# Optimization experiments

Measured on AMD Instinct MI355X. Metric: run time of the kernel, lower is better.

Reference implementation:

```python
import jax, jax.numpy as jnp
import numpy as np

D_MODEL = 1024
SCALE = 1.0 / np.sqrt(D_MODEL)


def setup_inputs() -> dict:
    key = jax.random.key(0)
    ks = jax.random.split(key, 9)
    B, S, D = 4, 2048, D_MODEL
    std = 1.0 / np.sqrt(D)
    x = jax.random.normal(ks[0], (B, S, D), dtype=jnp.float32)
    # nn.Linear weights: [out, in]; we store transposed [in, out] for x @ W
    Wq = jax.random.uniform(ks[1], (D, D), jnp.float32, -std, std)
    bq = jax.random.uniform(ks[2], (D,), jnp.float32, -std, std)
    Wk = jax.random.uniform(ks[3], (D, D), jnp.float32, -std, std)
    bk = jax.random.uniform(ks[4], (D,), jnp.float32, -std, std)
    Wv = jax.random.uniform(ks[5], (D, D), jnp.float32, -std, std)
    bv = jax.random.uniform(ks[6], (D,), jnp.float32, -std, std)
    Wo = jax.random.uniform(ks[7], (D, D), jnp.float32, -std, std)
    bo = jax.random.uniform(ks[8], (D,), jnp.float32, -std, std)
    return {"x": x, "Wq": Wq, "bq": bq, "Wk": Wk, "bk": bk,
            "Wv": Wv, "bv": bv, "Wo": Wo, "bo": bo}


def reference(x, Wq, bq, Wk, bk, Wv, bv, Wo, bo):
    q = x @ Wq + bq                      # [B,S,D]
    k = x @ Wk + bk
    v = x @ Wv + bv
    scores = jnp.einsum('bsd,btd->bst', q, k) * SCALE  # [B,S,S]
    weights = jax.nn.softmax(scores, axis=-1)
    out = jnp.einsum('bst,btd->bsd', weights, v)       # [B,S,D]
    return out @ Wo + bo
```

## Files before the change

### kernel.cpp

```cpp
#include <hip/hip_runtime.h>
#include <hip/hip_bf16.h>
#include <cstdint>

typedef __bf16 bf16x8 __attribute__((ext_vector_type(8)));
typedef float f32x4 __attribute__((ext_vector_type(4)));

__device__ __forceinline__ float bf2f(unsigned short u) {
  union { unsigned int i; float f; } x; x.i = ((unsigned int)u) << 16; return x.f;
}
__device__ __forceinline__ unsigned short f2bf(float f) {
  __hip_bfloat16 h = __float2bfloat16(f);
  return __builtin_bit_cast(unsigned short, h);
}

__device__ __forceinline__ void gload_lds16(const void* g, void* l) {
  auto gp = reinterpret_cast<__attribute__((address_space(1))) char*>(
      reinterpret_cast<uintptr_t>(g));
  auto lp = reinterpret_cast<__attribute__((address_space(3))) char*>(
      reinterpret_cast<uintptr_t>(l));
  __builtin_amdgcn_global_load_lds(gp, lp, 16, 0, 0);
}

#define SB() __builtin_amdgcn_sched_barrier(0)
#define BAR()                         \
  do {                                \
    SB();                             \
    __builtin_amdgcn_s_barrier();     \
    SB();                             \
  } while (0)
#define LGKM0()                                          \
  do {                                                   \
    asm volatile("s_waitcnt lgkmcnt(0)" ::: "memory");   \
    SB();                                                \
  } while (0)

__device__ __forceinline__ void xcd_swz(int& bx, int& by, int& bz) {
  const int gx = gridDim.x, gy = gridDim.y;
  const int n = gx * gy * (int)gridDim.z;
  int lin = blockIdx.x + gx * (blockIdx.y + gy * blockIdx.z);
  lin = (lin & 7) * (n >> 3) + (lin >> 3);
  bx = lin % gx; lin /= gx;
  by = lin % gy; bz = lin / gy;
}

__global__ __launch_bounds__(256) void cvt_f32_to_bf16(
    const float* __restrict__ in, unsigned short* __restrict__ out, long n4) {
  long i = (long)blockIdx.x * 256 + threadIdx.x;
  if (i >= n4) return;
  const float4 v = reinterpret_cast<const float4*>(in)[i];
  ushort4 o;
  o.x = f2bf(v.x); o.y = f2bf(v.y); o.z = f2bf(v.z); o.w = f2bf(v.w);
  reinterpret_cast<ushort4*>(out)[i] = o;
}

__global__ void transpose_w4(const float* __restrict__ w0,
                             const float* __restrict__ w1,
                             const float* __restrict__ w2,
                             const float* __restrict__ w3,
                             unsigned short* __restrict__ out) {
  const int z = blockIdx.z;
  const float* in = (z == 0) ? w0 : (z == 1) ? w1 : (z == 2) ? w2 : w3;
  out += (size_t)z * 1024 * 1024;
  __shared__ float tile[32][33];
  const int c0 = blockIdx.x * 32, r0 = blockIdx.y * 32;
  tile[threadIdx.y][threadIdx.x] =
      in[(size_t)(r0 + threadIdx.y) * 1024 + c0 + threadIdx.x];
  __syncthreads();
  out[(size_t)(c0 + threadIdx.y) * 1024 + r0 + threadIdx.x] =
      f2bf(tile[threadIdx.x][threadIdx.y]);
}

__global__ void concat_bias3(const float* a, const float* b, const float* c,
                             float* o) {
  int i = blockIdx.x * 256 + threadIdx.x;
  if (i >= 3072) return;
  o[i] = (i < 1024) ? a[i] : (i < 2048 ? b[i - 1024] : c[i - 2048]);
}

#define STAGE128(gbase, ld, ldsbase, rowbase)                                 \
  {                                                                           \
    _Pragma("unroll") for (int l_ = 0; l_ < 2; ++l_) {                        \
      const int seg_ = (w << 1) + l_;                                         \
      const int r0_ = (rowbase) + (seg_ << 3);                                \
      const int gr_ = r0_ + (lane >> 3);                                      \
      const int sc_ = ((lane & 7) ^ (lane >> 3)) << 3;                        \
      gload_lds16((gbase) + (size_t)gr_ * (ld) + sc_, (ldsbase) + r0_ * 64);  \
    }                                                                         \
  }

#define LDA_FRAG(dst, tile, rbase)                                            \
  _Pragma("unroll") for (int m_ = 0; m_ < 4; ++m_)                            \
  _Pragma("unroll") for (int kk_ = 0; kk_ < 2; ++kk_) {                       \
    const int row_ = (rbase) + (m_ << 4) + (lane & 15);                       \
    const int ch_ = ((kk_ << 2) + (lane >> 4)) ^ (lane & 7);                  \
    dst[m_][kk_] =                                                            \
        *reinterpret_cast<const bf16x8*>((tile) + row_ * 64 + (ch_ << 3));    \
  }
#define LDB_FRAG(dst, tile, rbase)                                            \
  _Pragma("unroll") for (int n_ = 0; n_ < 2; ++n_)                            \
  _Pragma("unroll") for (int kk_ = 0; kk_ < 2; ++kk_) {                       \
    const int row_ = (rbase) + (n_ << 4) + (lane & 15);                       \
    const int ch_ = ((kk_ << 2) + (lane >> 4)) ^ (lane & 7);                  \
    dst[n_][kk_] =                                                            \
        *reinterpret_cast<const bf16x8*>((tile) + row_ * 64 + (ch_ << 3));    \
  }

#define STAGE_A(gbase, ld, ldsbase, h)                                        \
  {                                                                           \
    _Pragma("unroll") for (int l_ = 0; l_ < 2; ++l_) {                        \
      const int seg_ = (w << 1) + l_;                                         \
      const int r0_ = ((seg_ >> 3) << 7) + ((h) << 6) + ((seg_ & 7) << 3);    \
      const int gr_ = r0_ + (lane >> 3);                                      \
      const int sc_ = ((lane & 7) ^ (lane >> 3)) << 3;                        \
      gload_lds16((gbase) + (size_t)gr_ * (ld) + sc_, (ldsbase) + r0_ * 64);  \
    }                                                                         \
  }
#define STAGE_B(gbase, ld, ldsbase, h)                                        \
  {                                                                           \
    _Pragma("unroll") for (int l_ = 0; l_ < 2; ++l_) {                        \
      const int seg_ = (w << 1) + l_;                                         \
      const int r0_ = ((seg_ >> 2) << 6) + ((h) << 5) + ((seg_ & 3) << 3);    \
      const int gr_ = r0_ + (lane >> 3);                                      \
      const int sc_ = ((lane & 7) ^ (lane >> 3)) << 3;                        \
      gload_lds16((gbase) + (size_t)gr_ * (ld) + sc_, (ldsbase) + r0_ * 64);  \
    }                                                                         \
  }

#define MFMA_QUAD(a_, b_, af_, bf_)                                           \
  __builtin_amdgcn_s_setprio(1);                                              \
  _Pragma("unroll") for (int m_ = 0; m_ < 4; ++m_)                            \
  _Pragma("unroll") for (int n_ = 0; n_ < 2; ++n_)                            \
  _Pragma("unroll") for (int kk_ = 0; kk_ < 2; ++kk_)                         \
      acc[(a_) * 4 + m_][(b_) * 2 + n_] =                                     \
          __builtin_amdgcn_mfma_f32_16x16x32_bf16(                            \
              af_[m_][kk_], bf_[n_][kk_], acc[(a_) * 4 + m_][(b_) * 2 + n_],  \
              0, 0, 0);                                                       \
  __builtin_amdgcn_s_setprio(0);

template <typename OutT, bool HAS_BIAS>
__global__ __launch_bounds__(512, 2) void gemm256(
    const unsigned short* __restrict__ A,
    const unsigned short* __restrict__ Bt,
    OutT* __restrict__ C,
    const float* __restrict__ bias,
    int K, int lda, int ldb, int ldc, float scale,
    long sA, long sB, long sC) {
  int bx, by, bz;
  xcd_swz(bx, by, bz);
  A  += (long)bz * sA;
  Bt += (long)bz * sB;
  C  += (long)bz * sC;
  const int n0 = bx << 8;
  const int m0 = by << 8;
  __shared__ __attribute__((aligned(16))) unsigned short lds[2 * 32768];
  const int t = threadIdx.x;
  const int lane = t & 63;
  const int w = t >> 6;
  const int wm = w >> 2, wn = w & 3;
  const unsigned short* gA = A + (size_t)m0 * lda;
  const unsigned short* gB = Bt + (size_t)n0 * ldb;
  const int NT = K >> 6;

  f32x4 acc[8][4];
  const f32x4 vz = {0.f, 0.f, 0.f, 0.f};
#pragma unroll
  for (int i = 0; i < 8; ++i)
#pragma unroll
    for (int j = 0; j < 4; ++j) acc[i][j] = vz;

  {
    unsigned short* a0 = lds;
    unsigned short* b0t = lds + 16384;
    STAGE_A(gA, lda, a0, 0);
    STAGE_B(gB, ldb, b0t, 0);
    STAGE_B(gB, ldb, b0t, 1);
    STAGE_A(gA, lda, a0, 1);
    if (NT > 1) {
      unsigned short* a1 = lds + 32768;
      unsigned short* b1t = lds + 32768 + 16384;
      STAGE_A(gA + 64, lda, a1, 0);
      STAGE_B(gB + 64, ldb, b1t, 0);
      STAGE_B(gB + 64, ldb, b1t, 1);
      asm volatile("s_waitcnt vmcnt(6)" ::: "memory");
    } else {
      asm volatile("s_waitcnt vmcnt(0)" ::: "memory");
    }
  }
  BAR();

  for (int kt = 0; kt < NT; ++kt) {
    unsigned short* at = lds + ((kt & 1) << 15);
    unsigned short* bt = at + 16384;
    unsigned short* atN = lds + (((kt + 1) & 1) << 15);
    const unsigned short* gA1 = gA + (size_t)(kt + 1) * 64;
    const unsigned short* gA2 = gA + (size_t)(kt + 2) * 64;
    const unsigned short* gB2 = gB + (size_t)(kt + 2) * 64;
    const bool st1 = kt + 1 < NT, st2 = kt + 2 < NT;

    bf16x8 af[4][2], b0[2][2], b1[2][2];

    LDA_FRAG(af, at, (wm << 7));
    LDB_FRAG(b0, bt, (wn << 6));
    if (st1) STAGE_A(gA1, lda, atN, 1);
    BAR();
    LGKM0();
    MFMA_QUAD(0, 0, af, b0);
    BAR();

    LDB_FRAG(b1, bt, (wn << 6) + 32);
    if (st2) STAGE_A(gA2, lda, at, 0);
    BAR();
    LGKM0();
    MFMA_QUAD(0, 1, af, b1);
    BAR();

    LDA_FRAG(af, at, (wm << 7) + 64);
    if (st2) STAGE_B(gB2, ldb, bt, 0);
    BAR();
    LGKM0();
    MFMA_QUAD(1, 0, af, b0);
    BAR();

    if (st2) STAGE_B(gB2, ldb, bt, 1);
    if (kt < NT - 3) {
      asm volatile("s_waitcnt vmcnt(6)" ::: "memory");
    } else {
      asm volatile("s_waitcnt vmcnt(0)" ::: "memory");
    }
    BAR();
    MFMA_QUAD(1, 1, af, b1);
    BAR();
  }

  const int crow0 = m0 + (wm << 7) + ((lane >> 4) << 2);
  const int ccol0 = n0 + (wn << 6) + (lane & 15);
#pragma unroll
  for (int mf = 0; mf < 8; ++mf) {
#pragma unroll
    for (int nf = 0; nf < 4; ++nf) {
      const int col = ccol0 + (nf << 4);
      const float bb = HAS_BIAS ? bias[col] : 0.f;
#pragma unroll
      for (int i = 0; i < 4; ++i) {
        const int row = crow0 + (mf << 4) + i;
        const float v = acc[mf][nf][i] * scale + bb;
        if constexpr (sizeof(OutT) == 2) {
          C[(size_t)row * ldc + col] = (OutT)f2bf(v);
        } else {
          C[(size_t)row * ldc + col] = (OutT)v;
        }
      }
    }
  }
}

#define MFMA_QUAD128(b_, af_, bf_)                                            \
  __builtin_amdgcn_s_setprio(1);                                              \
  _Pragma("unroll") for (int m_ = 0; m_ < 4; ++m_)                            \
  _Pragma("unroll") for (int n_ = 0; n_ < 2; ++n_)                            \
  _Pragma("unroll") for (int kk_ = 0; kk_ < 2; ++kk_)                         \
      acc[m_][(b_) * 2 + n_] = __builtin_amdgcn_mfma_f32_16x16x32_bf16(       \
          af_[m_][kk_], bf_[n_][kk_], acc[m_][(b_) * 2 + n_], 0, 0, 0);       \
  __builtin_amdgcn_s_setprio(0);

template <typename OutT, bool HAS_BIAS, bool VSPLIT>
__global__ __launch_bounds__(512, 2) void gemm128t(
    const unsigned short* __restrict__ A,
    const unsigned short* __restrict__ Bt,
    OutT* __restrict__ C,
    const float* __restrict__ bias,
    unsigned short* __restrict__ vt,
    int K, int lda, int ldb, int ldc, float scale,
    long sA, long sB, long sC) {
  int bx, by, bz;
  xcd_swz(bx, by, bz);
  A  += (long)bz * sA;
  Bt += (long)bz * sB;
  C  += (long)bz * sC;
  const int n0 = bx << 7;
  const int m0 = by << 8;
  __shared__ __attribute__((aligned(16))) unsigned short lds[3 * 24576];
  const int t = threadIdx.x;
  const int lane = t & 63;
  const int w = t >> 6;
  const int wm = w >> 1, wn = w & 1;
  const unsigned short* gA = A + (size_t)m0 * lda;
  const unsigned short* gB = Bt + (size_t)n0 * ldb;
  const int NT = K >> 6;

  f32x4 acc[4][4];
  const f32x4 vz = {0.f, 0.f, 0.f, 0.f};
#pragma unroll
  for (int i = 0; i < 4; ++i)
#pragma unroll
    for (int j = 0; j < 4; ++j) acc[i][j] = vz;

  {
    STAGE128(gA, lda, lds, 0);
    STAGE128(gA, lda, lds, 128);
    STAGE128(gB, ldb, lds + 16384, 0);
    STAGE128(gA + 64, lda, lds + 24576, 0);
    STAGE128(gA + 64, lda, lds + 24576, 128);
    STAGE128(gB + 64, ldb, lds + 24576 + 16384, 0);
    asm volatile("s_waitcnt vmcnt(6)" ::: "memory");
  }
  BAR();

  int idx = 0;
  for (int kt = 0; kt < NT; ++kt) {
    unsigned short* at = lds + idx * 24576;
    unsigned short* btile = at + 16384;
    int idx2 = idx + 2; if (idx2 >= 3) idx2 -= 3;
    unsigned short* st = lds + idx2 * 24576;
    const unsigned short* gA2 = gA + (size_t)(kt + 2) * 64;
    const unsigned short* gB2 = gB + (size_t)(kt + 2) * 64;
    const bool st2 = kt + 2 < NT;

    bf16x8 af[4][2], b0[2][2], b1[2][2];

    LDA_FRAG(af, at, (wm << 6));
    LDB_FRAG(b0, btile, (wn << 6));
    if (st2) {
      STAGE128(gA2, lda, st, 0);
      STAGE128(gA2, lda, st, 128);
    }
    BAR();
    LGKM0();
    MFMA_QUAD128(0, af, b0);
    BAR();

    LDB_FRAG(b1, btile, (wn << 6) + 32);
    if (st2) STAGE128(gB2, ldb, st + 16384, 0);
    if (kt < NT - 2) {
      asm volatile("s_waitcnt vmcnt(6)" ::: "memory");
    } else {
      asm volatile("s_waitcnt vmcnt(0)" ::: "memory");
    }
    BAR();
    LGKM0();
    MFMA_QUAD128(1, af, b1);
    BAR();

    idx = (idx + 1 == 3) ? 0 : idx + 1;
  }

  const int crow0 = m0 + (wm << 6) + ((lane >> 4) << 2);
  const int ccol0 = n0 + (wn << 6) + (lane & 15);

  if (VSPLIT && n0 >= 2048) {
    const int b = m0 >> 11;
#pragma unroll
    for (int mf = 0; mf < 4; ++mf) {
#pragma unroll
      for (int nf = 0; nf < 4; ++nf) {
        const int col = ccol0 + (nf << 4);
        const float bb = HAS_BIAS ? bias[col] : 0.f;
        const int d = col - 2048;
        const int s = (crow0 & 2047) + (mf << 4);
        ushort4 o;
        o.x = f2bf(acc[mf][nf][0] * scale + bb);
        o.y = f2bf(acc[mf][nf][1] * scale + bb);
        o.z = f2bf(acc[mf][nf][2] * scale + bb);
        o.w = f2bf(acc[mf][nf][3] * scale + bb);
        *reinterpret_cast<ushort4*>(vt + (((size_t)b << 10) + d) * 2048 + s) = o;
      }
    }
    return;
  }

#pragma unroll
  for (int mf = 0; mf < 4; ++mf) {
#pragma unroll
    for (int nf = 0; nf < 4; ++nf) {
      const int col = ccol0 + (nf << 4);
      const float bb = HAS_BIAS ? bias[col] : 0.f;
#pragma unroll
      for (int i = 0; i < 4; ++i) {
        const int row = crow0 + (mf << 4) + i;
        const float v = acc[mf][nf][i] * scale + bb;
        if constexpr (sizeof(OutT) == 2) {
          C[(size_t)row * ldc + col] = (OutT)f2bf(v);
        } else {
          C[(size_t)row * ldc + col] = (OutT)v;
        }
      }
    }
  }
}

__global__ __launch_bounds__(256) void softmax_inplace(
    unsigned short* __restrict__ P, int S) {
  const size_t row = blockIdx.x;
  unsigned short* p = P + row * (size_t)S;
  const int t = threadIdx.x;
  const int lane = t & 63, w = t >> 6;
  const uint4 raw = reinterpret_cast<const uint4*>(p)[t];
  unsigned int u[4] = {raw.x, raw.y, raw.z, raw.w};
  float v[8];
#pragma unroll
  for (int j = 0; j < 4; ++j) {
    v[2 * j]     = bf2f((unsigned short)(u[j] & 0xffffu));
    v[2 * j + 1] = bf2f((unsigned short)(u[j] >> 16));
  }
  float mx = v[0];
#pragma unroll
  for (int j = 1; j < 8; ++j) mx = fmaxf(mx, v[j]);
#pragma unroll
  for (int off = 32; off >= 1; off >>= 1) mx = fmaxf(mx, __shfl_xor(mx, off, 64));
  __shared__ float red[4];
  if (lane == 0) red[w] = mx;
  __syncthreads();
  mx = fmaxf(fmaxf(red[0], red[1]), fmaxf(red[2], red[3]));
  float e[8];
  float s = 0.f;
#pragma unroll
  for (int j = 0; j < 8; ++j) { e[j] = __expf(v[j] - mx); s += e[j]; }
#pragma unroll
  for (int off = 32; off >= 1; off >>= 1) s += __shfl_xor(s, off, 64);
  __syncthreads();
  if (lane == 0) red[w] = s;
  __syncthreads();
  s = red[0] + red[1] + red[2] + red[3];
  const float inv = 1.f / s;
  unsigned int o[4];
#pragma unroll
  for (int j = 0; j < 4; ++j)
    o[j] = (unsigned int)f2bf(e[2 * j] * inv) |
           ((unsigned int)f2bf(e[2 * j + 1] * inv) << 16);
  uint4 ov; ov.x = o[0]; ov.y = o[1]; ov.z = o[2]; ov.w = o[3];
  reinterpret_cast<uint4*>(p)[t] = ov;
}

extern "C" void kernel_launch(void* const* d_in, const int* in_sizes, int n_in,
                              void* d_out, int out_size, void* d_ws, size_t ws_size,
                              hipStream_t stream) {
  (void)in_sizes; (void)n_in; (void)out_size; (void)ws_size;
  const float* x  = (const float*)d_in[0];
  const float* Wq = (const float*)d_in[1];
  const float* bq = (const float*)d_in[2];
  const float* Wk = (const float*)d_in[3];
  const float* bk = (const float*)d_in[4];
  const float* Wv = (const float*)d_in[5];
  const float* bv = (const float*)d_in[6];
  const float* Wo = (const float*)d_in[7];
  const float* bo = (const float*)d_in[8];
  float* out = (float*)d_out;

  constexpr int B = 4, S = 2048, D = 1024;
  constexpr long BS = (long)B * S;
  constexpr size_t MB = 1ull << 20;
  char* ws = (char*)d_ws;
  unsigned short* xb   = (unsigned short*)(ws + 0);
  unsigned short* Wall = (unsigned short*)(ws + 16 * MB);
  float*          bqkv = (float*)(ws + 24 * MB);
  unsigned short* QKVc = (unsigned short*)(ws + 25 * MB);
  unsigned short* Vt   = (unsigned short*)(ws + 57 * MB);
  unsigned short* Sc   = (unsigned short*)(ws + 73 * MB);
  unsigned short* AO   = (unsigned short*)(ws + 0);

  const float scale = 0.03125f;

  cvt_f32_to_bf16<<<(BS * D / 4 + 255) / 256, 256, 0, stream>>>(x, xb, BS * D / 4);
  transpose_w4<<<dim3(32, 32, 4), dim3(32, 32), 0, stream>>>(Wq, Wk, Wv, Wo, Wall);
  concat_bias3<<<12, 256, 0, stream>>>(bq, bk, bv, bqkv);

  gemm128t<unsigned short, true, true><<<dim3(24, 32, 1), 512, 0, stream>>>(
      xb, Wall, QKVc, bqkv, Vt, D, D, D, 2048, 1.f, 0, 0, 0);

  gemm256<unsigned short, false><<<dim3(S / 256, S / 256, B), 512, 0, stream>>>(
      QKVc + 0, QKVc + 1024, Sc, nullptr, D, 2048, 2048, S, scale,
      (long)S * 2048, (long)S * 2048, (long)S * S);

  softmax_inplace<<<B * S, 256, 0, stream>>>(Sc, S);

  gemm128t<unsigned short, false, false><<<dim3(8, 8, 4), 512, 0, stream>>>(
      Sc, Vt, AO, nullptr, nullptr, S, S, S, D, 1.f,
      (long)S * S, (long)D * S, (long)S * D);

  gemm128t<float, true, false><<<dim3(8, 32, 1), 512, 0, stream>>>(
      AO, Wall + 3 * 1024 * 1024, out, bo, nullptr, D, D, D, D, 1.f, 0, 0, 0);
}
```

Before: 205.1 us.

## Use persistent 256-tile GEMM with cross-tile prefetch for QKV and scores

Adds a persistent 256x256 GEMM kernel launched with 256 workgroups. Each workgroup loops over several output tiles and prefetches the next tile's K-slices while finishing the current one, which hides the pipeline ramp at tile boundaries and covers tail effects. The QKV projection now uses this kernel in place of the 128-tile kernel, and the fused V-transpose epilogue is replaced by a separate bf16 transpose kernel. MFMA operands are swapped so each lane holds four consecutive columns, allowing vectorized float4/ushort4 stores with vector bias loads. The trade-offs are an extra kernel launch with its own memory round trip for the V transpose, and a fixed assumption of K=1024 (16 K-steps per tile).

```diff
diff --git a/kernel.cpp b/kernel.cpp
--- a/kernel.cpp
+++ b/kernel.cpp
@@ -70,6 +70,20 @@
       f2bf(tile[threadIdx.x][threadIdx.y]);
 }
 
+__global__ void transpose_bf16(const unsigned short* __restrict__ in,
+                               unsigned short* __restrict__ out,
+                               int ldIn, int ldOut, long sIn, long sOut) {
+  in  += (long)blockIdx.z * sIn;
+  out += (long)blockIdx.z * sOut;
+  __shared__ unsigned short tile[32][33];
+  const int c0 = blockIdx.x * 32, r0 = blockIdx.y * 32;
+  tile[threadIdx.y][threadIdx.x] =
+      in[(size_t)(r0 + threadIdx.y) * ldIn + c0 + threadIdx.x];
+  __syncthreads();
+  out[(size_t)(c0 + threadIdx.y) * ldOut + r0 + threadIdx.x] =
+      tile[threadIdx.x][threadIdx.y];
+}
+
 __global__ void concat_bias3(const float* a, const float* b, const float* c,
                              float* o) {
   int i = blockIdx.x * 256 + threadIdx.x;
@@ -87,24 +101,6 @@
       gload_lds16((gbase) + (size_t)gr_ * (ld) + sc_, (ldsbase) + r0_ * 64);  \
     }                                                                         \
   }
-
-#define LDA_FRAG(dst, tile, rbase)                                            \
-  _Pragma("unroll") for (int m_ = 0; m_ < 4; ++m_)                            \
-  _Pragma("unroll") for (int kk_ = 0; kk_ < 2; ++kk_) {                       \
-    const int row_ = (rbase) + (m_ << 4) + (lane & 15);                       \
-    const int ch_ = ((kk_ << 2) + (lane >> 4)) ^ (lane & 7);                  \
-    dst[m_][kk_] =                                                            \
-        *reinterpret_cast<const bf16x8*>((tile) + row_ * 64 + (ch_ << 3));    \
-  }
-#define LDB_FRAG(dst, tile, rbase)                                            \
-  _Pragma("unroll") for (int n_ = 0; n_ < 2; ++n_)                            \
-  _Pragma("unroll") for (int kk_ = 0; kk_ < 2; ++kk_) {                       \
-    const int row_ = (rbase) + (n_ << 4) + (lane & 15);                       \
-    const int ch_ = ((kk_ << 2) + (lane >> 4)) ^ (lane & 7);                  \
-    dst[n_][kk_] =                                                            \
-        *reinterpret_cast<const bf16x8*>((tile) + row_ * 64 + (ch_ << 3));    \
-  }
-
 #define STAGE_A(gbase, ld, ldsbase, h)                                        \
   {                                                                           \
     _Pragma("unroll") for (int l_ = 0; l_ < 2; ++l_) {                        \
@@ -126,6 +122,23 @@
     }                                                                         \
   }
 
+#define LDA_FRAG(dst, tile, rbase)                                            \
+  _Pragma("unroll") for (int m_ = 0; m_ < 4; ++m_)                            \
+  _Pragma("unroll") for (int kk_ = 0; kk_ < 2; ++kk_) {                       \
+    const int row_ = (rbase) + (m_ << 4) + (lane & 15);                       \
+    const int ch_ = ((kk_ << 2) + (lane >> 4)) ^ (lane & 7);                  \
+    dst[m_][kk_] =                                                            \
+        *reinterpret_cast<const bf16x8*>((tile) + row_ * 64 + (ch_ << 3));    \
+  }
+#define LDB_FRAG(dst, tile, rbase)                                            \
+  _Pragma("unroll") for (int n_ = 0; n_ < 2; ++n_)                            \
+  _Pragma("unroll") for (int kk_ = 0; kk_ < 2; ++kk_) {                       \
+    const int row_ = (rbase) + (n_ << 4) + (lane & 15);                       \
+    const int ch_ = ((kk_ << 2) + (lane >> 4)) ^ (lane & 7);                  \
+    dst[n_][kk_] =                                                            \
+        *reinterpret_cast<const bf16x8*>((tile) + row_ * 64 + (ch_ << 3));    \
+  }
+
 #define MFMA_QUAD(a_, b_, af_, bf_)                                           \
   __builtin_amdgcn_s_setprio(1);                                              \
   _Pragma("unroll") for (int m_ = 0; m_ < 4; ++m_)                            \
@@ -133,126 +146,9 @@
   _Pragma("unroll") for (int kk_ = 0; kk_ < 2; ++kk_)                         \
       acc[(a_) * 4 + m_][(b_) * 2 + n_] =                                     \
           __builtin_amdgcn_mfma_f32_16x16x32_bf16(                            \
-              af_[m_][kk_], bf_[n_][kk_], acc[(a_) * 4 + m_][(b_) * 2 + n_],  \
+              bf_[n_][kk_], af_[m_][kk_], acc[(a_) * 4 + m_][(b_) * 2 + n_],  \
               0, 0, 0);                                                       \
   __builtin_amdgcn_s_setprio(0);
-
-template <typename OutT, bool HAS_BIAS>
-__global__ __launch_bounds__(512, 2) void gemm256(
-    const unsigned short* __restrict__ A,
-    const unsigned short* __restrict__ Bt,
-    OutT* __restrict__ C,
-    const float* __restrict__ bias,
-    int K, int lda, int ldb, int ldc, float scale,
-    long sA, long sB, long sC) {
-  int bx, by, bz;
-  xcd_swz(bx, by, bz);
-  A  += (long)bz * sA;
-  Bt += (long)bz * sB;
-  C  += (long)bz * sC;
-  const int n0 = bx << 8;
-  const int m0 = by << 8;
-  __shared__ __attribute__((aligned(16))) unsigned short lds[2 * 32768];
-  const int t = threadIdx.x;
-  const int lane = t & 63;
-  const int w = t >> 6;
-  const int wm = w >> 2, wn = w & 3;
-  const unsigned short* gA = A + (size_t)m0 * lda;
-  const unsigned short* gB = Bt + (size_t)n0 * ldb;
-  const int NT = K >> 6;
-
-  f32x4 acc[8][4];
-  const f32x4 vz = {0.f, 0.f, 0.f, 0.f};
-#pragma unroll
-  for (int i = 0; i < 8; ++i)
-#pragma unroll
-    for (int j = 0; j < 4; ++j) acc[i][j] = vz;
-
-  {
-    unsigned short* a0 = lds;
-    unsigned short* b0t = lds + 16384;
-    STAGE_A(gA, lda, a0, 0);
-    STAGE_B(gB, ldb, b0t, 0);
-    STAGE_B(gB, ldb, b0t, 1);
-    STAGE_A(gA, lda, a0, 1);
-    if (NT > 1) {
-      unsigned short* a1 = lds + 32768;
-      unsigned short* b1t = lds + 32768 + 16384;
-      STAGE_A(gA + 64, lda, a1, 0);
-      STAGE_B(gB + 64, ldb, b1t, 0);
-      STAGE_B(gB + 64, ldb, b1t, 1);
-      asm volatile("s_waitcnt vmcnt(6)" ::: "memory");
-    } else {
-      asm volatile("s_waitcnt vmcnt(0)" ::: "memory");
-    }
-  }
-  BAR();
-
-  for (int kt = 0; kt < NT; ++kt) {
-    unsigned short* at = lds + ((kt & 1) << 15);
-    unsigned short* bt = at + 16384;
-    unsigned short* atN = lds + (((kt + 1) & 1) << 15);
-    const unsigned short* gA1 = gA + (size_t)(kt + 1) * 64;
-    const unsigned short* gA2 = gA + (size_t)(kt + 2) * 64;
-    const unsigned short* gB2 = gB + (size_t)(kt + 2) * 64;
-    const bool st1 = kt + 1 < NT, st2 = kt + 2 < NT;
-
-    bf16x8 af[4][2], b0[2][2], b1[2][2];
-
-    LDA_FRAG(af, at, (wm << 7));
-    LDB_FRAG(b0, bt, (wn << 6));
-    if (st1) STAGE_A(gA1, lda, atN, 1);
-    BAR();
-    LGKM0();
-    MFMA_QUAD(0, 0, af, b0);
-    BAR();
-
-    LDB_FRAG(b1, bt, (wn << 6) + 32);
-    if (st2) STAGE_A(gA2, lda, at, 0);
-    BAR();
-    LGKM0();
-    MFMA_QUAD(0, 1, af, b1);
-    BAR();
-
-    LDA_FRAG(af, at, (wm << 7) + 64);
-    if (st2) STAGE_B(gB2, ldb, bt, 0);
-    BAR();
-    LGKM0();
-    MFMA_QUAD(1, 0, af, b0);
-    BAR();
-
-    if (st2) STAGE_B(gB2, ldb, bt, 1);
-    if (kt < NT - 3) {
-      asm volatile("s_waitcnt vmcnt(6)" ::: "memory");
-    } else {
-      asm volatile("s_waitcnt vmcnt(0)" ::: "memory");
-    }
-    BAR();
-    MFMA_QUAD(1, 1, af, b1);
-    BAR();
-  }
-
-  const int crow0 = m0 + (wm << 7) + ((lane >> 4) << 2);
-  const int ccol0 = n0 + (wn << 6) + (lane & 15);
-#pragma unroll
-  for (int mf = 0; mf < 8; ++mf) {
-#pragma unroll
-    for (int nf = 0; nf < 4; ++nf) {
-      const int col = ccol0 + (nf << 4);
-      const float bb = HAS_BIAS ? bias[col] : 0.f;
-#pragma unroll
-      for (int i = 0; i < 4; ++i) {
-        const int row = crow0 + (mf << 4) + i;
-        const float v = acc[mf][nf][i] * scale + bb;
-        if constexpr (sizeof(OutT) == 2) {
-          C[(size_t)row * ldc + col] = (OutT)f2bf(v);
-        } else {
-          C[(size_t)row * ldc + col] = (OutT)v;
-        }
-      }
-    }
-  }
-}
 
 #define MFMA_QUAD128(b_, af_, bf_)                                            \
   __builtin_amdgcn_s_setprio(1);                                              \
@@ -260,16 +156,172 @@
   _Pragma("unroll") for (int n_ = 0; n_ < 2; ++n_)                            \
   _Pragma("unroll") for (int kk_ = 0; kk_ < 2; ++kk_)                         \
       acc[m_][(b_) * 2 + n_] = __builtin_amdgcn_mfma_f32_16x16x32_bf16(       \
-          af_[m_][kk_], bf_[n_][kk_], acc[m_][(b_) * 2 + n_], 0, 0, 0);       \
+          bf_[n_][kk_], af_[m_][kk_], acc[m_][(b_) * 2 + n_], 0, 0, 0);       \
   __builtin_amdgcn_s_setprio(0);
 
-template <typename OutT, bool HAS_BIAS, bool VSPLIT>
+template <typename OutT, bool HAS_BIAS>
+__global__ __launch_bounds__(512, 2) void gemm256p(
+    const unsigned short* __restrict__ A,
+    const unsigned short* __restrict__ Bt,
+    OutT* __restrict__ C,
+    const float* __restrict__ bias,
+    int lda, int ldb, int ldc, float scale,
+    int tilesTotal, int tx, int txy,
+    long sA, long sB, long sC) {
+  const int gphys = blockIdx.x;
+  const int g = ((gphys & 7) << 5) + (gphys >> 3);
+  __shared__ __attribute__((aligned(16))) unsigned short lds[2 * 32768];
+  const int t = threadIdx.x;
+  const int lane = t & 63;
+  const int w = t >> 6;
+  const int wm = w >> 2, wn = w & 3;
+
+  const int ntb = (tilesTotal - g + 255) >> 8;
+  const int myTotK = ntb << 4;
+
+  int jj = g;
+  int m0c = ((jj % txy) / tx) << 8;
+  int n0c = (jj % tx) << 8;
+  const unsigned short* gAc = A + (long)(jj / txy) * sA + (size_t)m0c * lda;
+  const unsigned short* gBc = Bt + (long)(jj / txy) * sB + (size_t)n0c * ldb;
+  OutT* Cc = C + (long)(jj / txy) * sC;
+  int jn = jj + 256;
+  const unsigned short* gAn = gAc;
+  const unsigned short* gBn = gBc;
+  if (jn < tilesTotal) {
+    gAn = A + (long)(jn / txy) * sA + (size_t)(((jn % txy) / tx) << 8) * lda;
+    gBn = Bt + (long)(jn / txy) * sB + (size_t)((jn % tx) << 8) * ldb;
+  }
+
+  f32x4 acc[8][4];
+  const f32x4 vz = {0.f, 0.f, 0.f, 0.f};
+#pragma unroll
+  for (int i = 0; i < 8; ++i)
+#pragma unroll
+    for (int j = 0; j < 4; ++j) acc[i][j] = vz;
+
+  {
+    unsigned short* a0 = lds;
+    unsigned short* b0t = lds + 16384;
+    STAGE_A(gAc, lda, a0, 0);
+    STAGE_B(gBc, ldb, b0t, 0);
+    STAGE_B(gBc, ldb, b0t, 1);
+    STAGE_A(gAc, lda, a0, 1);
+    if (myTotK > 1) {
+      unsigned short* a1 = lds + 32768;
+      unsigned short* b1t = lds + 32768 + 16384;
+      STAGE_A(gAc + 64, lda, a1, 0);
+      STAGE_B(gBc + 64, ldb, b1t, 0);
+      STAGE_B(gBc + 64, ldb, b1t, 1);
+      asm volatile("s_waitcnt vmcnt(6)" ::: "memory");
+    } else {
+      asm volatile("s_waitcnt vmcnt(0)" ::: "memory");
+    }
+  }
+  BAR();
+
+  for (int kg = 0; kg < myTotK; ++kg) {
+    const int kt = kg & 15;
+    unsigned short* at = lds + ((kg & 1) << 15);
+    unsigned short* bt = at + 16384;
+    unsigned short* atN = lds + (((kg + 1) & 1) << 15);
+    const unsigned short* pA1 = (kt < 15) ? gAc + (size_t)(kt + 1) * 64 : gAn;
+    const unsigned short* pA2 =
+        (kt < 14) ? gAc + (size_t)(kt + 2) * 64 : gAn + (size_t)(kt - 14) * 64;
+    const unsigned short* pB2 =
+        (kt < 14) ? gBc + (size_t)(kt + 2) * 64 : gBn + (size_t)(kt - 14) * 64;
+    const bool s1 = kg + 1 < myTotK, s2 = kg + 2 < myTotK;
+
+    bf16x8 af[4][2], b0[2][2], b1[2][2];
+
+    LDA_FRAG(af, at, (wm << 7));
+    LDB_FRAG(b0, bt, (wn << 6));
+    if (s1) STAGE_A(pA1, lda, atN, 1);
+    BAR();
+    LGKM0();
+    MFMA_QUAD(0, 0, af, b0);
+    BAR();
+
+    LDB_FRAG(b1, bt, (wn << 6) + 32);
+    if (s2) STAGE_A(pA2, lda, at, 0);
+    BAR();
+    LGKM0();
+    MFMA_QUAD(0, 1, af, b1);
+    BAR();
+
+    LDA_FRAG(af, at, (wm << 7) + 64);
+    if (s2) STAGE_B(pB2, ldb, bt, 0);
+    BAR();
+    LGKM0();
+    MFMA_QUAD(1, 0, af, b0);
+    BAR();
+
+    if (s2) STAGE_B(pB2, ldb, bt, 1);
+    if (kg < myTotK - 3) {
+      asm volatile("s_waitcnt vmcnt(6)" ::: "memory");
+    } else {
+      asm volatile("s_waitcnt vmcnt(0)" ::: "memory");
+    }
+    BAR();
+    MFMA_QUAD(1, 1, af, b1);
+    BAR();
+
+    if (kt == 15) {
+      const int mrow0 = m0c + (wm << 7) + (lane & 15);
+      const int ncol0 = n0c + (wn << 6) + ((lane >> 4) << 2);
+#pragma unroll
+      for (int mf = 0; mf < 8; ++mf) {
+        const int row = mrow0 + (mf << 4);
+#pragma unroll
+        for (int nf = 0; nf < 4; ++nf) {
+          const int col = ncol0 + (nf << 4);
+          float4 bb = {0.f, 0.f, 0.f, 0.f};
+          if (HAS_BIAS) bb = *reinterpret_cast<const float4*>(bias + col);
+          const f32x4 a = acc[mf][nf];
+          if constexpr (sizeof(OutT) == 2) {
+            ushort4 o;
+            o.x = f2bf(a[0] * scale + bb.x);
+            o.y = f2bf(a[1] * scale + bb.y);
+            o.z = f2bf(a[2] * scale + bb.z);
+            o.w = f2bf(a[3] * scale + bb.w);
+            *reinterpret_cast<ushort4*>(&Cc[(size_t)row * ldc + col]) = o;
+          } else {
+            float4 o;
+            o.x = a[0] * scale + bb.x;
+            o.y = a[1] * scale + bb.y;
+            o.z = a[2] * scale + bb.z;
+            o.w = a[3] * scale + bb.w;
+            *reinterpret_cast<float4*>(&Cc[(size_t)row * ldc + col]) = o;
+          }
+        }
+      }
+      if (kg + 1 < myTotK) {
+        jj = jn;
+        m0c = ((jj % txy) / tx) << 8;
+        n0c = (jj % tx) << 8;
+        gAc = gAn;
+        gBc = gBn;
+        Cc = C + (long)(jj / txy) * sC;
+        jn = jj + 256;
+        if (jn < tilesTotal) {
+          gAn = A + (long)(jn / txy) * sA + (size_t)(((jn % txy) / tx) << 8) * lda;
+          gBn = Bt + (long)(jn / txy) * sB + (size_t)((jn % tx) << 8) * ldb;
+        }
+#pragma unroll
+        for (int i = 0; i < 8; ++i)
+#pragma unroll
+          for (int j = 0; j < 4; ++j) acc[i][j] = vz;
+      }
+    }
+  }
+}
+
+template <typename OutT, bool HAS_BIAS>
 __global__ __launch_bounds__(512, 2) void gemm128t(
     const unsigned short* __restrict__ A,
     const unsigned short* __restrict__ Bt,
     OutT* __restrict__ C,
     const float* __restrict__ bias,
-    unsigned short* __restrict__ vt,
     int K, int lda, int ldb, int ldc, float scale,
     long sA, long sB, long sC) {
   int bx, by, bz;
@@ -344,45 +396,31 @@
     idx = (idx + 1 == 3) ? 0 : idx + 1;
   }
 
-  const int crow0 = m0 + (wm << 6) + ((lane >> 4) << 2);
-  const int ccol0 = n0 + (wn << 6) + (lane & 15);
-
-  if (VSPLIT && n0 >= 2048) {
-    const int b = m0 >> 11;
-#pragma unroll
-    for (int mf = 0; mf < 4; ++mf) {
-#pragma unroll
-      for (int nf = 0; nf < 4; ++nf) {
-        const int col = ccol0 + (nf << 4);
-        const float bb = HAS_BIAS ? bias[col] : 0.f;
-        const int d = col - 2048;
-        const int s = (crow0 & 2047) + (mf << 4);
+  const int mrow0 = m0 + (wm << 6) + (lane & 15);
+  const int ncol0 = n0 + (wn << 6) + ((lane >> 4) << 2);
+#pragma unroll
+  for (int mf = 0; mf < 4; ++mf) {
+    const int row = mrow0 + (mf << 4);
+#pragma unroll
+    for (int nf = 0; nf < 4; ++nf) {
+      const int col = ncol0 + (nf << 4);
+      float4 bb = {0.f, 0.f, 0.f, 0.f};
+      if (HAS_BIAS) bb = *reinterpret_cast<const float4*>(bias + col);
+      const f32x4 a = acc[mf][nf];
+      if constexpr (sizeof(OutT) == 2) {
         ushort4 o;
-        o.x = f2bf(acc[mf][nf][0] * scale + bb);
-        o.y = f2bf(acc[mf][nf][1] * scale + bb);
-        o.z = f2bf(acc[mf][nf][2] * scale + bb);
-        o.w = f2bf(acc[mf][nf][3] * scale + bb);
-        *reinterpret_cast<ushort4*>(vt + (((size_t)b << 10) + d) * 2048 + s) = o;
-      }
-    }
-    return;
-  }
-
-#pragma unroll
-  for (int mf = 0; mf < 4; ++mf) {
-#pragma unroll
-    for (int nf = 0; nf < 4; ++nf) {
-      const int col = ccol0 + (nf << 4);
-      const float bb = HAS_BIAS ? bias[col] : 0.f;
-#pragma unroll
-      for (int i = 0; i < 4; ++i) {
-        const int row = crow0 + (mf << 4) + i;
-        const float v = acc[mf][nf][i] * scale + bb;
-        if constexpr (sizeof(OutT) == 2) {
-          C[(size_t)row * ldc + col] = (OutT)f2bf(v);
-        } else {
-          C[(size_t)row * ldc + col] = (OutT)v;
-        }
+        o.x = f2bf(a[0] * scale + bb.x);
+        o.y = f2bf(a[1] * scale + bb.y);
+        o.z = f2bf(a[2] * scale + bb.z);
+        o.w = f2bf(a[3] * scale + bb.w);
+        *reinterpret_cast<ushort4*>(&C[(size_t)row * ldc + col]) = o;
+      } else {
+        float4 o;
+        o.x = a[0] * scale + bb.x;
+        o.y = a[1] * scale + bb.y;
+        o.z = a[2] * scale + bb.z;
+        o.w = a[3] * scale + bb.w;
+        *reinterpret_cast<float4*>(&C[(size_t)row * ldc + col]) = o;
       }
     }
   }
@@ -454,8 +492,8 @@
   unsigned short* Wall = (unsigned short*)(ws + 16 * MB);
   float*          bqkv = (float*)(ws + 24 * MB);
   unsigned short* QKVc = (unsigned short*)(ws + 25 * MB);
-  unsigned short* Vt   = (unsigned short*)(ws + 57 * MB);
   unsigned short* Sc   = (unsigned short*)(ws + 73 * MB);
+  unsigned short* Vt   = (unsigned short*)(ws + 105 * MB);
   unsigned short* AO   = (unsigned short*)(ws + 0);
 
   const float scale = 0.03125f;
@@ -464,19 +502,22 @@
   transpose_w4<<<dim3(32, 32, 4), dim3(32, 32), 0, stream>>>(Wq, Wk, Wv, Wo, Wall);
   concat_bias3<<<12, 256, 0, stream>>>(bq, bk, bv, bqkv);
 
-  gemm128t<unsigned short, true, true><<<dim3(24, 32, 1), 512, 0, stream>>>(
-      xb, Wall, QKVc, bqkv, Vt, D, D, D, 2048, 1.f, 0, 0, 0);
-
-  gemm256<unsigned short, false><<<dim3(S / 256, S / 256, B), 512, 0, stream>>>(
-      QKVc + 0, QKVc + 1024, Sc, nullptr, D, 2048, 2048, S, scale,
-      (long)S * 2048, (long)S * 2048, (long)S * S);
+  gemm256p<unsigned short, true><<<256, 512, 0, stream>>>(
+      xb, Wall, QKVc, bqkv, D, D, 3072, 1.f, 384, 12, 384, 0, 0, 0);
+
+  transpose_bf16<<<dim3(32, 64, 4), dim3(32, 32), 0, stream>>>(
+      QKVc + 2048, Vt, 3072, S, (long)S * 3072, (long)D * S);
+
+  gemm256p<unsigned short, false><<<256, 512, 0, stream>>>(
+      QKVc + 0, QKVc + 1024, Sc, nullptr, 3072, 3072, S, scale,
+      256, 8, 64, (long)S * 3072, (long)S * 3072, (long)S * S);
 
   softmax_inplace<<<B * S, 256, 0, stream>>>(Sc, S);
 
-  gemm128t<unsigned short, false, false><<<dim3(8, 8, 4), 512, 0, stream>>>(
-      Sc, Vt, AO, nullptr, nullptr, S, S, S, D, 1.f,
+  gemm128t<unsigned short, false><<<dim3(8, 8, 4), 512, 0, stream>>>(
+      Sc, Vt, AO, nullptr, S, S, S, D, 1.f,
       (long)S * S, (long)D * S, (long)S * D);
 
-  gemm128t<float, true, false><<<dim3(8, 32, 1), 512, 0, stream>>>(
-      AO, Wall + 3 * 1024 * 1024, out, bo, nullptr, D, D, D, D, 1.f, 0, 0, 0);
-}
+  gemm128t<float, true><<<dim3(8, 32, 1), 512, 0, stream>>>(
+      AO, Wall + 3 * 1024 * 1024, out, bo, D, D, D, D, 1.f, 0, 0, 0);
+}
```

Measured after the change: 231.0 us. 12.6% more time.
